# Kernel tuning notes

Measured on AMD Instinct MI355X. Metric: run time of the kernel, lower is better.

Reference implementation:

```python
import jax, jax.numpy as jnp
import numpy as np

B, N, C, H = 1, 4096, 768, 12
HD = C // H  # 64
EPS = 1e-5


def _rope_freqs(n, hd, theta=10000.0):
    inv = 1.0 / (theta ** (np.arange(0, hd, 2, dtype=np.float32) / hd))  # (hd/2,)
    ang = np.outer(np.arange(n, dtype=np.float32), inv)  # (N, hd/2)
    return jnp.asarray(np.cos(ang)), jnp.asarray(np.sin(ang))


def setup_inputs() -> dict:
    key = jax.random.key(0)
    ks = jax.random.split(key, 5)
    cos, sin = _rope_freqs(N, HD)
    s = lambda d: 1.0 / np.sqrt(d)
    return {
        "x": jax.random.normal(ks[0], (B, N, C), jnp.float32),
        "freqs_cos": cos,
        "freqs_sin": sin,
        "w_qkv": jax.random.normal(ks[1], (3 * C, C), jnp.float32) * s(C),
        "w_proj": jax.random.normal(ks[2], (C, C), jnp.float32) * s(C),
        "b_proj": jnp.zeros((C,), jnp.float32),
        "g1": jnp.ones((C,), jnp.float32),
        "beta1": jnp.zeros((C,), jnp.float32),
        "g2": jnp.ones((C,), jnp.float32),
        "beta2": jnp.zeros((C,), jnp.float32),
        "w_fc1": jax.random.normal(ks[3], (4 * C, C), jnp.float32) * s(C),
        "b_fc1": jnp.zeros((4 * C,), jnp.float32),
        "w_fc2": jax.random.normal(ks[4], (C, 4 * C), jnp.float32) * s(4 * C),
        "b_fc2": jnp.zeros((C,), jnp.float32),
    }


def _layernorm(x, g, b):
    mu = jnp.mean(x, -1, keepdims=True)
    var = jnp.mean(jnp.square(x - mu), -1, keepdims=True)
    return (x - mu) * jax.lax.rsqrt(var + EPS) * g + b


def _apply_rope(t, cos, sin):
    # t: (B, N, H, HD); cos/sin: (N, HD/2) -> broadcast (1, N, 1, HD/2)
    t = t.reshape(*t.shape[:-1], HD // 2, 2)
    t0, t1 = t[..., 0], t[..., 1]
    c = cos[None, :, None, :]
    s = sin[None, :, None, :]
    out = jnp.stack([t0 * c - t1 * s, t0 * s + t1 * c], axis=-1)
    return out.reshape(*out.shape[:-2], HD)


def reference(x, freqs_cos, freqs_sin, w_qkv, w_proj, b_proj, g1, beta1, g2, beta2,
              w_fc1, b_fc1, w_fc2, b_fc2):
    # --- attention branch ---
    h = _layernorm(x, g1, beta1)
    qkv = (h @ w_qkv.T).reshape(B, N, 3, H, HD)
    q, k, v = qkv[:, :, 0], qkv[:, :, 1], qkv[:, :, 2]  # (B,N,H,HD)
    q = _apply_rope(q, freqs_cos, freqs_sin)
    k = _apply_rope(k, freqs_cos, freqs_sin)
    scale = HD ** (-0.5)
    attn = jnp.einsum('bnhd,bmhd->bhnm', q, k) * scale
    attn = jax.nn.softmax(attn, axis=-1)
    o = jnp.einsum('bhnm,bmhd->bnhd', attn, v).reshape(B, N, C)
    x = x + o @ w_proj.T + b_proj
    # --- mlp branch ---
    h = _layernorm(x, g2, beta2)
    h = jax.nn.gelu(h @ w_fc1.T + b_fc1, approximate=False)
    x = x + h @ w_fc2.T + b_fc2
    return x
```

## Files before the change

### kernel.cpp

```cpp
#include <hip/hip_runtime.h>
#include <hip/hip_bf16.h>
#include <math.h>

#define LOG2E 1.44269504088896340736f

typedef short bf16x8 __attribute__((ext_vector_type(8)));
typedef float f32x4 __attribute__((ext_vector_type(4)));

static __device__ __forceinline__ float bf2f(ushort u){
  union { float f; unsigned int u; } x; x.u = ((unsigned int)u) << 16; return x.f;
}
static __device__ __forceinline__ ushort f2bf(float f){
  union { float f; unsigned int u; } x; x.f = f;
  unsigned int r = x.u + 0x7fffu + ((x.u >> 16) & 1u);
  return (ushort)(r >> 16);
}
static __device__ __forceinline__ unsigned cvt_pk_bf16(float a, float b){
  unsigned r;
  asm("v_cvt_pk_bf16_f32 %0, %1, %2" : "=v"(r) : "v"(a), "v"(b));
  return r;
}
static __device__ __forceinline__ float fmax3(float a, float b, float c){
  return fmaxf(fmaxf(a, b), c);
}
static __device__ __forceinline__ void gload_lds16(const void* g, void* l){
  __builtin_amdgcn_global_load_lds(
      (const __attribute__((address_space(1))) unsigned int*)g,
      (__attribute__((address_space(3))) unsigned int*)l, 16, 0, 0);
}

__global__ __launch_bounds__(256) void cvt_f32_bf16(const float* __restrict__ src,
                                                    ushort* __restrict__ dst, int n4){
  int i = blockIdx.x * 256 + threadIdx.x;
  if (i < n4){
    float4 v = ((const float4*)src)[i];
    ushort4 o;
    o.x = f2bf(v.x); o.y = f2bf(v.y); o.z = f2bf(v.z); o.w = f2bf(v.w);
    ((ushort4*)dst)[i] = o;
  }
}

__device__ __forceinline__ float block_sum256(float s, float* red){
  #pragma unroll
  for (int off = 32; off; off >>= 1) s += __shfl_xor(s, off, 64);
  int w = threadIdx.x >> 6;
  if ((threadIdx.x & 63) == 0) red[w] = s;
  __syncthreads();
  float tot = red[0] + red[1] + red[2] + red[3];
  __syncthreads();
  return tot;
}

__global__ __launch_bounds__(256) void ln_kernel(const float* __restrict__ x,
                                                 const float* __restrict__ g,
                                                 const float* __restrict__ bta,
                                                 ushort* __restrict__ out){
  __shared__ float red[4];
  int row = blockIdx.x, t = threadIdx.x;
  const float* xr = x + (size_t)row * 768;
  float v0 = xr[t], v1 = xr[t + 256], v2 = xr[t + 512];
  float mu = block_sum256(v0 + v1 + v2, red) * (1.0f / 768.0f);
  float d0 = v0 - mu, d1 = v1 - mu, d2 = v2 - mu;
  float var = block_sum256(d0*d0 + d1*d1 + d2*d2, red) * (1.0f / 768.0f);
  float rs = rsqrtf(var + 1e-5f);
  ushort* orow = out + (size_t)row * 768;
  orow[t]       = f2bf(d0 * rs * g[t]       + bta[t]);
  orow[t + 256] = f2bf(d1 * rs * g[t + 256] + bta[t + 256]);
  orow[t + 512] = f2bf(d2 * rs * g[t + 512] + bta[t + 512]);
}

template<int MODE>
__global__ __launch_bounds__(256) void gemm_bf16(const ushort* __restrict__ A, int lda,
                                                 const ushort* __restrict__ Bm, int ldb,
                                                 int K,
                                                 const float* __restrict__ bias,
                                                 const float* __restrict__ res, int ldr,
                                                 void* __restrict__ out, int ldo){
  __shared__ __align__(16) ushort As[128 * 64];
  __shared__ __align__(16) ushort Bs[128 * 64];
  const int tid = threadIdx.x;
  const int m0 = blockIdx.x * 128, n0 = blockIdx.y * 128;
  const int w = tid >> 6, l = tid & 63;
  const int wm = (w >> 1) * 64, wn = (w & 1) * 64;
  const int lr = l & 15, lg = l >> 4;
  const int lane8 = l >> 3, sl = l & 7;
  const int koff = (MODE == 3) ? blockIdx.z * K : 0;

  f32x4 acc[4][4] = {};

  for (int k0 = 0; k0 < K; k0 += 64){
    #pragma unroll
    for (int j = 0; j < 4; ++j){
      int instr = w * 4 + j;
      int row = instr * 8 + lane8;
      gload_lds16((const char*)A + ((size_t)(m0 + row) * lda + koff + k0) * 2 + ((sl ^ (row & 7)) << 4),
                  (char*)As + instr * 1024);
      gload_lds16((const char*)Bm + ((size_t)(n0 + row) * ldb + koff + k0) * 2 + ((sl ^ (row & 7)) << 4),
                  (char*)Bs + instr * 1024);
    }
    __syncthreads();
    #pragma unroll
    for (int kk = 0; kk < 2; ++kk){
      bf16x8 af[4], bfr[4];
      #pragma unroll
      for (int mi = 0; mi < 4; ++mi){
        int row = wm + mi * 16 + lr;
        int cg = (kk * 4 + lg) ^ (row & 7);
        af[mi] = *(const bf16x8*)(As + row * 64 + cg * 8);
      }
      #pragma unroll
      for (int nj = 0; nj < 4; ++nj){
        int row = wn + nj * 16 + lr;
        int cg = (kk * 4 + lg) ^ (row & 7);
        bfr[nj] = *(const bf16x8*)(Bs + row * 64 + cg * 8);
      }
      #pragma unroll
      for (int mi = 0; mi < 4; ++mi)
        #pragma unroll
        for (int nj = 0; nj < 4; ++nj)
          acc[mi][nj] = __builtin_amdgcn_mfma_f32_16x16x32_bf16(af[mi], bfr[nj], acc[mi][nj], 0, 0, 0);
    }
    __syncthreads();
  }

  const size_t zout = (MODE == 3) ? (size_t)blockIdx.z * gridDim.x * 128 * ldo : 0;

  #pragma unroll
  for (int mi = 0; mi < 4; ++mi){
    #pragma unroll
    for (int nj = 0; nj < 4; ++nj){
      #pragma unroll
      for (int r = 0; r < 4; ++r){
        int grow = m0 + wm + mi * 16 + lg * 4 + r;
        int gcol = n0 + wn + nj * 16 + lr;
        float v = acc[mi][nj][r];
        if (MODE == 0){
          ((ushort*)out)[(size_t)grow * ldo + gcol] = f2bf(v);
        } else if (MODE == 1){
          v += bias[gcol] + res[(size_t)grow * ldr + gcol];
          ((float*)out)[(size_t)grow * ldo + gcol] = v;
        } else if (MODE == 2){
          v += bias[gcol];
          v = 0.5f * v * (1.0f + erff(v * 0.70710678118654752f));
          ((ushort*)out)[(size_t)grow * ldo + gcol] = f2bf(v);
        } else {
          ((float*)out)[zout + (size_t)grow * ldo + gcol] = v;
        }
      }
    }
  }
}

__global__ __launch_bounds__(192) void gemm_combine4(const float* __restrict__ parts,
                                                     const float* __restrict__ bias,
                                                     const float* __restrict__ res,
                                                     float* __restrict__ out){
  int q = blockIdx.x, t = threadIdx.x;
  size_t idx = (size_t)q * 768 + t * 4;
  const size_t seg = (size_t)4096 * 768;
  f32x4 o = *(const f32x4*)(parts + idx);
  #pragma unroll
  for (int s = 1; s < 4; ++s) o += *(const f32x4*)(parts + s * seg + idx);
  f32x4 b = *(const f32x4*)(bias + t * 4);
  f32x4 rr = *(const f32x4*)(res + idx);
  o += b + rr;
  *(f32x4*)(out + idx) = o;
}

__global__ __launch_bounds__(384) void rope_kernel(const ushort* __restrict__ qkv,
                                                   const float* __restrict__ fc,
                                                   const float* __restrict__ fs,
                                                   ushort* __restrict__ Qs,
                                                   ushort* __restrict__ Ks,
                                                   ushort* __restrict__ Vt){
  int n = blockIdx.x, t = threadIdx.x;
  int h = t >> 5, p = t & 31;
  float c = fc[(size_t)n * 32 + p], s = fs[(size_t)n * 32 + p];
  const ushort* row = qkv + (size_t)n * 2304;
  const float qscale = 0.125f * LOG2E;
  {
    float t0 = bf2f(row[h * 64 + 2 * p]), t1 = bf2f(row[h * 64 + 2 * p + 1]);
    ushort* dst = Qs + ((size_t)h * 4096 + n) * 64;
    dst[2 * p]     = f2bf((t0 * c - t1 * s) * qscale);
    dst[2 * p + 1] = f2bf((t0 * s + t1 * c) * qscale);
  }
  {
    float t0 = bf2f(row[768 + h * 64 + 2 * p]), t1 = bf2f(row[768 + h * 64 + 2 * p + 1]);
    ushort* dst = Ks + ((size_t)h * 4096 + n) * 64;
    dst[2 * p]     = f2bf(t0 * c - t1 * s);
    dst[2 * p + 1] = f2bf(t0 * s + t1 * c);
  }
  #pragma unroll
  for (int i = 0; i < 2; ++i){
    int idx = t + i * 384;
    int hh = idx >> 6, d = idx & 63;
    Vt[((size_t)hh * 64 + d) * 4096 + n] = row[1536 + idx];
  }
}

__global__ __launch_bounds__(256, 4) void flash_attn(const ushort* __restrict__ Qs,
                                                     const ushort* __restrict__ Ks,
                                                     const ushort* __restrict__ Vt,
                                                     float* __restrict__ Opart,
                                                     float* __restrict__ Ml){
  __shared__ __align__(16) char smem[32768];
  const int h = blockIdx.y, kh = blockIdx.z;
  const int w = threadIdx.x >> 6, l = threadIdx.x & 63;
  const int lr = l & 15, lg = l >> 4;
  const int lane8 = l >> 3, sl = l & 7;
  const int q0 = blockIdx.x * 128 + w * 32;
  const ushort* Qh = Qs + (size_t)h * (4096 * 64);
  const char* Kh = (const char*)(Ks + (size_t)h * (4096 * 64));
  const char* Vh = (const char*)(Vt + (size_t)h * (64 * 4096));

  bf16x8 qa[2][2];
  #pragma unroll
  for (int qf = 0; qf < 2; ++qf)
    #pragma unroll
    for (int kk = 0; kk < 2; ++kk)
      qa[qf][kk] = *(const bf16x8*)(Qh + (size_t)(q0 + qf * 16 + lr) * 64 + kk * 32 + lg * 8);

  const char* kbase = Kh + (size_t)(kh * 1024 + w * 16 + lane8) * 128;
  const char* vbase = Vh + (size_t)(w * 16 + lane8) * 8192 + kh * 2048 + ((sl ^ lane8) << 4);
  int koff[2];
  #pragma unroll
  for (int j = 0; j < 2; ++j)
    koff[j] = j * 1024 + ((sl ^ ((lane8 & 3) | (((w * 2 + j) & 1) << 2))) << 4);

  const int a_ = lr >> 2, b_ = lr & 3;
  const int krow = 8 * a_ + b_;
  const int f_ = b_ | ((a_ & 1) << 2);
  const int kslot0 = (lg ^ f_) << 4;
  const int kslot1 = ((4 + lg) ^ f_) << 4;
  const int vslot0 = lr * 128 + ((lg ^ (lr & 7)) << 4);
  const int vslot1 = lr * 128 + (((4 + lg) ^ (lr & 7)) << 4);

  f32x4 oacc[2][4] = {};
  f32x4 lacc[2] = {};
  float m_prev[2] = {0.0f, 0.0f};
  union { unsigned u[4]; bf16x8 v; } ones;
  #pragma unroll
  for (int i = 0; i < 4; ++i) ones.u[i] = 0x3F803F80u;

  auto stage = [&](int tile, char* Kb, char* Vb){
    #pragma unroll
    for (int j = 0; j < 2; ++j){
      gload_lds16(kbase + (size_t)tile * 8192 + koff[j], Kb + (w * 2 + j) * 1024);
      gload_lds16(vbase + (size_t)j * 65536 + (size_t)tile * 128, Vb + (w * 2 + j) * 1024);
    }
  };

  auto compute = [&](const char* Kb, const char* Vb, bool first){
    #pragma unroll
    for (int kk = 0; kk < 2; ++kk){
      const bool fst = first && (kk == 0);
      f32x4 sh[2][2];
      #pragma unroll
      for (int qf = 0; qf < 2; ++qf){
        float iv = fst ? 0.0f : -m_prev[qf];
        #pragma unroll
        for (int tt = 0; tt < 2; ++tt){
          sh[qf][tt][0] = iv; sh[qf][tt][1] = iv; sh[qf][tt][2] = iv; sh[qf][tt][3] = iv;
        }
      }
      #pragma unroll
      for (int tt = 0; tt < 2; ++tt){
        const char* kr = Kb + (krow + 4 * tt + 32 * kk) * 128;
        bf16x8 k0 = *(const bf16x8*)(kr + kslot0);
        bf16x8 k1 = *(const bf16x8*)(kr + kslot1);
        #pragma unroll
        for (int qf = 0; qf < 2; ++qf){
          sh[qf][tt] = __builtin_amdgcn_mfma_f32_16x16x32_bf16(k0, qa[qf][0], sh[qf][tt], 0, 0, 0);
          sh[qf][tt] = __builtin_amdgcn_mfma_f32_16x16x32_bf16(k1, qa[qf][1], sh[qf][tt], 0, 0, 0);
        }
      }
      float mb[2];
      #pragma unroll
      for (int qf = 0; qf < 2; ++qf){
        float m1 = fmax3(sh[qf][0][0], sh[qf][0][1], sh[qf][0][2]);
        float m2 = fmax3(sh[qf][0][3], sh[qf][1][0], sh[qf][1][1]);
        float m3 = fmaxf(sh[qf][1][2], sh[qf][1][3]);
        float mm = fmax3(m1, m2, m3);
        mm = fmaxf(mm, __shfl_xor(mm, 16, 64));
        mm = fmaxf(mm, __shfl_xor(mm, 32, 64));
        mb[qf] = mm;
      }
      if (fst){
        #pragma unroll
        for (int qf = 0; qf < 2; ++qf){
          m_prev[qf] = mb[qf];
          #pragma unroll
          for (int tt = 0; tt < 2; ++tt)
            #pragma unroll
            for (int r = 0; r < 4; ++r) sh[qf][tt][r] -= mb[qf];
        }
      } else if (!__all(mb[0] <= 8.0f && mb[1] <= 8.0f)){
        #pragma unroll
        for (int qf = 0; qf < 2; ++qf){
          float d = (mb[qf] > 8.0f) ? mb[qf] : 0.0f;
          float sc = exp2f(-d);
          #pragma unroll
          for (int tt = 0; tt < 2; ++tt)
            #pragma unroll
            for (int r = 0; r < 4; ++r) sh[qf][tt][r] -= d;
          #pragma unroll
          for (int db = 0; db < 4; ++db)
            #pragma unroll
            for (int r = 0; r < 4; ++r) oacc[qf][db][r] *= sc;
          #pragma unroll
          for (int r = 0; r < 4; ++r) lacc[qf][r] *= sc;
          m_prev[qf] += d;
        }
      }
      #pragma unroll
      for (int qf = 0; qf < 2; ++qf)
        #pragma unroll
        for (int tt = 0; tt < 2; ++tt)
          #pragma unroll
          for (int r = 0; r < 4; ++r)
            sh[qf][tt][r] = exp2f(sh[qf][tt][r]);
      union { unsigned u[4]; bf16x8 v; } pf[2];
      #pragma unroll
      for (int qf = 0; qf < 2; ++qf){
        pf[qf].u[0] = cvt_pk_bf16(sh[qf][0][0], sh[qf][0][1]);
        pf[qf].u[1] = cvt_pk_bf16(sh[qf][0][2], sh[qf][0][3]);
        pf[qf].u[2] = cvt_pk_bf16(sh[qf][1][0], sh[qf][1][1]);
        pf[qf].u[3] = cvt_pk_bf16(sh[qf][1][2], sh[qf][1][3]);
      }
      const int vs = kk ? vslot1 : vslot0;
      #pragma unroll
      for (int db = 0; db < 4; ++db){
        bf16x8 vf = *(const bf16x8*)(Vb + vs + db * 2048);
        #pragma unroll
        for (int qf = 0; qf < 2; ++qf)
          oacc[qf][db] = __builtin_amdgcn_mfma_f32_16x16x32_bf16(vf, pf[qf].v, oacc[qf][db], 0, 0, 0);
      }
      #pragma unroll
      for (int qf = 0; qf < 2; ++qf)
        lacc[qf] = __builtin_amdgcn_mfma_f32_16x16x32_bf16(ones.v, pf[qf].v, lacc[qf], 0, 0, 0);
    }
  };

  char* K0 = smem;          char* V0 = smem + 8192;
  char* K1 = smem + 16384;  char* V1 = smem + 24576;

  stage(0, K0, V0);
  __syncthreads();
  stage(1, K1, V1);
  compute(K0, V0, true);
  __syncthreads();
  stage(2, K0, V0);
  compute(K1, V1, false);
  __syncthreads();
  #pragma unroll 1
  for (int it2 = 1; it2 < 8; ++it2){
    stage(2 * it2 + 1, K1, V1);
    compute(K0, V0, false);
    __syncthreads();
    if (it2 < 7) stage(2 * it2 + 2, K0, V0);
    compute(K1, V1, false);
    __syncthreads();
  }

  #pragma unroll
  for (int qf = 0; qf < 2; ++qf){
    int q = q0 + qf * 16 + lr;
    float* Op = Opart + ((size_t)(kh * 12 + h) * 4096 + q) * 64;
    #pragma unroll
    for (int db = 0; db < 4; ++db)
      *(f32x4*)(Op + db * 16 + 4 * lg) = oacc[qf][db];
    if (lg == 0){
      float2 ml; ml.x = m_prev[qf]; ml.y = lacc[qf][0];
      *(float2*)(Ml + ((size_t)(kh * 12 + h) * 4096 + q) * 2) = ml;
    }
  }
}

__global__ __launch_bounds__(192) void attn_combine(const float* __restrict__ Opart,
                                                    const float* __restrict__ Ml,
                                                    ushort* __restrict__ O){
  int q = blockIdx.x, t = threadIdx.x;
  int h = t >> 4;
  float2 ml[4];
  float m = -1e30f;
  #pragma unroll
  for (int s = 0; s < 4; ++s){
    ml[s] = *(const float2*)(Ml + ((size_t)(s * 12 + h) * 4096 + q) * 2);
    m = fmaxf(m, ml[s].x);
  }
  float wgt[4], lsum = 0.0f;
  #pragma unroll
  for (int s = 0; s < 4; ++s){
    wgt[s] = exp2f(ml[s].x - m);
    lsum += ml[s].y * wgt[s];
  }
  float inv = 1.0f / lsum;
  int dd = (t & 15) * 4;
  f32x4 o = {};
  #pragma unroll
  for (int s = 0; s < 4; ++s){
    f32x4 os = *(const f32x4*)(Opart + ((size_t)(s * 12 + h) * 4096 + q) * 64 + dd);
    #pragma unroll
    for (int r = 0; r < 4; ++r) o[r] += os[r] * wgt[s];
  }
  uint2 ov;
  ov.x = cvt_pk_bf16(o[0] * inv, o[1] * inv);
  ov.y = cvt_pk_bf16(o[2] * inv, o[3] * inv);
  *(uint2*)(O + (size_t)q * 768 + t * 4) = ov;
}

extern "C" void kernel_launch(void* const* d_in, const int* in_sizes, int n_in,
                              void* d_out, int out_size, void* d_ws, size_t ws_size,
                              hipStream_t stream){
  const float* x      = (const float*)d_in[0];
  const float* fcos   = (const float*)d_in[1];
  const float* fsin   = (const float*)d_in[2];
  const float* w_qkv  = (const float*)d_in[3];
  const float* w_proj = (const float*)d_in[4];
  const float* b_proj = (const float*)d_in[5];
  const float* g1     = (const float*)d_in[6];
  const float* beta1  = (const float*)d_in[7];
  const float* g2     = (const float*)d_in[8];
  const float* beta2  = (const float*)d_in[9];
  const float* w_fc1  = (const float*)d_in[10];
  const float* b_fc1  = (const float*)d_in[11];
  const float* w_fc2  = (const float*)d_in[12];
  const float* b_fc2  = (const float*)d_in[13];

  char* ws = (char*)d_ws;
  size_t off = 0;
  auto alloc = [&](size_t bytes) -> char* {
    char* p = ws + off; off += (bytes + 255) & ~(size_t)255; return p;
  };
  ushort* wq  = (ushort*)alloc((size_t)2304 * 768 * 2);
  ushort* wp  = (ushort*)alloc((size_t)768 * 768 * 2);
  ushort* w1  = (ushort*)alloc((size_t)3072 * 768 * 2);
  ushort* w2  = (ushort*)alloc((size_t)768 * 3072 * 2);
  ushort* h1  = (ushort*)alloc((size_t)4096 * 768 * 2);
  ushort* qkv = (ushort*)alloc((size_t)4096 * 2304 * 2);
  ushort* Qs  = (ushort*)alloc((size_t)12 * 4096 * 64 * 2);
  ushort* Ks  = (ushort*)alloc((size_t)12 * 4096 * 64 * 2);
  ushort* Vt  = (ushort*)alloc((size_t)12 * 64 * 4096 * 2);
  ushort* ao  = (ushort*)alloc((size_t)4096 * 768 * 2);
  float*  x2  = (float*) alloc((size_t)4096 * 768 * 4);
  ushort* h2  = (ushort*)alloc((size_t)4096 * 768 * 2);
  ushort* f1  = (ushort*)alloc((size_t)4096 * 3072 * 2);
  float*  Opart = (float*)alloc((size_t)4 * 12 * 4096 * 64 * 4);
  float*  Ml    = (float*)alloc((size_t)4 * 12 * 4096 * 2 * 4);
  float*  skp   = Opart;

  cvt_f32_bf16<<<(2304*768/4 + 255)/256, 256, 0, stream>>>(w_qkv,  wq, 2304*768/4);
  cvt_f32_bf16<<<(768*768/4  + 255)/256, 256, 0, stream>>>(w_proj, wp, 768*768/4);
  cvt_f32_bf16<<<(3072*768/4 + 255)/256, 256, 0, stream>>>(w_fc1,  w1, 3072*768/4);
  cvt_f32_bf16<<<(768*3072/4 + 255)/256, 256, 0, stream>>>(w_fc2,  w2, 768*3072/4);

  ln_kernel<<<4096, 256, 0, stream>>>(x, g1, beta1, h1);
  gemm_bf16<0><<<dim3(32, 18), 256, 0, stream>>>(h1, 768, wq, 768, 768,
                                                 nullptr, nullptr, 0, qkv, 2304);
  rope_kernel<<<4096, 384, 0, stream>>>(qkv, fcos, fsin, Qs, Ks, Vt);
  flash_attn<<<dim3(32, 12, 4), 256, 0, stream>>>(Qs, Ks, Vt, Opart, Ml);
  attn_combine<<<4096, 192, 0, stream>>>(Opart, Ml, ao);
  gemm_bf16<3><<<dim3(32, 6, 4), 256, 0, stream>>>(ao, 768, wp, 768, 192,
                                                   nullptr, nullptr, 0, skp, 768);
  gemm_combine4<<<4096, 192, 0, stream>>>(skp, b_proj, x, x2);
  ln_kernel<<<4096, 256, 0, stream>>>(x2, g2, beta2, h2);
  gemm_bf16<2><<<dim3(32, 24), 256, 0, stream>>>(h2, 768, w1, 768, 768,
                                                 b_fc1, nullptr, 0, f1, 3072);
  gemm_bf16<3><<<dim3(32, 6, 4), 256, 0, stream>>>(f1, 3072, w2, 3072, 768,
                                                   nullptr, nullptr, 0, skp, 768);
  gemm_combine4<<<4096, 192, 0, stream>>>(skp, b_fc2, x2, (float*)d_out);
}
```

Before: 278.9 us.

## Fuse RoPE into QKV GEMM epilogue, merge weight casts, warp-per-row layernorm

The four weight conversion launches become one kernel. Layernorm now runs one row per wavefront with vector loads and no shared-memory reductions. The QKV GEMM gains an epilogue that applies RoPE through a DPP lane swap and writes Q, K and transposed V directly, so the separate rope kernel and the qkv intermediate buffer are gone. The output-projection GEMM drops split-K plus its combine pass and uses a fused bias-plus-residual epilogue. Flash attention computes the full 64-key score tile before a single max reduction, which halves the cross-lane reductions but keeps more registers live and launches fewer blocks for the projection.

```diff
diff --git a/kernel.cpp b/kernel.cpp
--- a/kernel.cpp
+++ b/kernel.cpp
@@ -23,50 +23,72 @@
 static __device__ __forceinline__ float fmax3(float a, float b, float c){
   return fmaxf(fmaxf(a, b), c);
 }
+static __device__ __forceinline__ float dpp_xor1(float v){
+  int i = __builtin_amdgcn_mov_dpp(__float_as_int(v), 0xB1, 0xF, 0xF, true);
+  return __int_as_float(i);
+}
 static __device__ __forceinline__ void gload_lds16(const void* g, void* l){
   __builtin_amdgcn_global_load_lds(
       (const __attribute__((address_space(1))) unsigned int*)g,
       (__attribute__((address_space(3))) unsigned int*)l, 16, 0, 0);
 }
 
-__global__ __launch_bounds__(256) void cvt_f32_bf16(const float* __restrict__ src,
-                                                    ushort* __restrict__ dst, int n4){
-  int i = blockIdx.x * 256 + threadIdx.x;
-  if (i < n4){
-    float4 v = ((const float4*)src)[i];
-    ushort4 o;
-    o.x = f2bf(v.x); o.y = f2bf(v.y); o.z = f2bf(v.z); o.w = f2bf(v.w);
-    ((ushort4*)dst)[i] = o;
-  }
-}
-
-__device__ __forceinline__ float block_sum256(float s, float* red){
-  #pragma unroll
-  for (int off = 32; off; off >>= 1) s += __shfl_xor(s, off, 64);
-  int w = threadIdx.x >> 6;
-  if ((threadIdx.x & 63) == 0) red[w] = s;
-  __syncthreads();
-  float tot = red[0] + red[1] + red[2] + red[3];
-  __syncthreads();
-  return tot;
+__global__ __launch_bounds__(256) void cvt_all(const float* __restrict__ s0, ushort* __restrict__ d0, int c0,
+                                               const float* __restrict__ s1, ushort* __restrict__ d1, int c1,
+                                               const float* __restrict__ s2, ushort* __restrict__ d2, int c2,
+                                               const float* __restrict__ s3, ushort* __restrict__ d3, int c3){
+  int j = blockIdx.x * 256 + threadIdx.x;
+  const float* s; ushort* d;
+  if (j < c0){ s = s0; d = d0; }
+  else { j -= c0;
+    if (j < c1){ s = s1; d = d1; }
+    else { j -= c1;
+      if (j < c2){ s = s2; d = d2; }
+      else { j -= c2; if (j >= c3) return; s = s3; d = d3; } } }
+  float4 v = ((const float4*)s)[j];
+  ushort4 o;
+  o.x = f2bf(v.x); o.y = f2bf(v.y); o.z = f2bf(v.z); o.w = f2bf(v.w);
+  ((ushort4*)d)[j] = o;
 }
 
 __global__ __launch_bounds__(256) void ln_kernel(const float* __restrict__ x,
                                                  const float* __restrict__ g,
                                                  const float* __restrict__ bta,
                                                  ushort* __restrict__ out){
-  __shared__ float red[4];
-  int row = blockIdx.x, t = threadIdx.x;
+  int w = threadIdx.x >> 6, l = threadIdx.x & 63;
+  int row = blockIdx.x * 4 + w;
   const float* xr = x + (size_t)row * 768;
-  float v0 = xr[t], v1 = xr[t + 256], v2 = xr[t + 512];
-  float mu = block_sum256(v0 + v1 + v2, red) * (1.0f / 768.0f);
-  float d0 = v0 - mu, d1 = v1 - mu, d2 = v2 - mu;
-  float var = block_sum256(d0*d0 + d1*d1 + d2*d2, red) * (1.0f / 768.0f);
-  float rs = rsqrtf(var + 1e-5f);
+  f32x4 v[3];
+  #pragma unroll
+  for (int i = 0; i < 3; ++i) v[i] = *(const f32x4*)(xr + i * 256 + l * 4);
+  float s = 0.0f;
+  #pragma unroll
+  for (int i = 0; i < 3; ++i)
+    #pragma unroll
+    for (int r = 0; r < 4; ++r) s += v[i][r];
+  #pragma unroll
+  for (int off = 32; off; off >>= 1) s += __shfl_xor(s, off, 64);
+  float mu = s * (1.0f / 768.0f);
+  float q = 0.0f;
+  #pragma unroll
+  for (int i = 0; i < 3; ++i)
+    #pragma unroll
+    for (int r = 0; r < 4; ++r){ float d = v[i][r] - mu; q += d * d; }
+  #pragma unroll
+  for (int off = 32; off; off >>= 1) q += __shfl_xor(q, off, 64);
+  float rs = rsqrtf(q * (1.0f / 768.0f) + 1e-5f);
   ushort* orow = out + (size_t)row * 768;
-  orow[t]       = f2bf(d0 * rs * g[t]       + bta[t]);
-  orow[t + 256] = f2bf(d1 * rs * g[t + 256] + bta[t + 256]);
-  orow[t + 512] = f2bf(d2 * rs * g[t + 512] + bta[t + 512]);
+  #pragma unroll
+  for (int i = 0; i < 3; ++i){
+    f32x4 gg = *(const f32x4*)(g + i * 256 + l * 4);
+    f32x4 bb = *(const f32x4*)(bta + i * 256 + l * 4);
+    ushort4 o;
+    o.x = f2bf((v[i][0] - mu) * rs * gg[0] + bb[0]);
+    o.y = f2bf((v[i][1] - mu) * rs * gg[1] + bb[1]);
+    o.z = f2bf((v[i][2] - mu) * rs * gg[2] + bb[2]);
+    o.w = f2bf((v[i][3] - mu) * rs * gg[3] + bb[3]);
+    *(ushort4*)(orow + i * 256 + l * 4) = o;
+  }
 }
 
 template<int MODE>
@@ -75,7 +97,12 @@
                                                  int K,
                                                  const float* __restrict__ bias,
                                                  const float* __restrict__ res, int ldr,
-                                                 void* __restrict__ out, int ldo){
+                                                 void* __restrict__ out, int ldo,
+                                                 const float* __restrict__ fc,
+                                                 const float* __restrict__ fs,
+                                                 ushort* __restrict__ Qs,
+                                                 ushort* __restrict__ Ks,
+                                                 ushort* __restrict__ Vt){
   __shared__ __align__(16) ushort As[128 * 64];
   __shared__ __align__(16) ushort Bs[128 * 64];
   const int tid = threadIdx.x;
@@ -124,6 +151,42 @@
   }
 
   const size_t zout = (MODE == 3) ? (size_t)blockIdx.z * gridDim.x * 128 * ldo : 0;
+
+  if (MODE == 4){
+    const int part = n0 / 768;
+    const float qsc = 0.125f * LOG2E;
+    #pragma unroll
+    for (int mi = 0; mi < 4; ++mi){
+      const int n_base = m0 + wm + mi * 16 + lg * 4;
+      #pragma unroll
+      for (int nj = 0; nj < 4; ++nj){
+        const int col = n0 + wn + nj * 16 + lr;
+        const int head = (col - part * 768) >> 6;
+        const int d = col & 63;
+        if (part == 2){
+          ushort4 pk;
+          pk.x = f2bf(acc[mi][nj][0]); pk.y = f2bf(acc[mi][nj][1]);
+          pk.z = f2bf(acc[mi][nj][2]); pk.w = f2bf(acc[mi][nj][3]);
+          *(ushort4*)(Vt + ((size_t)head * 64 + d) * 4096 + n_base) = pk;
+        } else {
+          const int p = d >> 1;
+          ushort* dst = (part == 0) ? Qs : Ks;
+          #pragma unroll
+          for (int r = 0; r < 4; ++r){
+            int n = n_base + r;
+            float v = acc[mi][nj][r];
+            float pv = dpp_xor1(v);
+            float c = fc[(size_t)n * 32 + p];
+            float sv = fs[(size_t)n * 32 + p];
+            float rr = v * c + pv * ((d & 1) ? sv : -sv);
+            if (part == 0) rr *= qsc;
+            dst[((size_t)head * 4096 + n) * 64 + d] = f2bf(rr);
+          }
+        }
+      }
+    }
+    return;
+  }
 
   #pragma unroll
   for (int mi = 0; mi < 4; ++mi){
@@ -167,37 +230,6 @@
   *(f32x4*)(out + idx) = o;
 }
 
-__global__ __launch_bounds__(384) void rope_kernel(const ushort* __restrict__ qkv,
-                                                   const float* __restrict__ fc,
-                                                   const float* __restrict__ fs,
-                                                   ushort* __restrict__ Qs,
-                                                   ushort* __restrict__ Ks,
-                                                   ushort* __restrict__ Vt){
-  int n = blockIdx.x, t = threadIdx.x;
-  int h = t >> 5, p = t & 31;
-  float c = fc[(size_t)n * 32 + p], s = fs[(size_t)n * 32 + p];
-  const ushort* row = qkv + (size_t)n * 2304;
-  const float qscale = 0.125f * LOG2E;
-  {
-    float t0 = bf2f(row[h * 64 + 2 * p]), t1 = bf2f(row[h * 64 + 2 * p + 1]);
-    ushort* dst = Qs + ((size_t)h * 4096 + n) * 64;
-    dst[2 * p]     = f2bf((t0 * c - t1 * s) * qscale);
-    dst[2 * p + 1] = f2bf((t0 * s + t1 * c) * qscale);
-  }
-  {
-    float t0 = bf2f(row[768 + h * 64 + 2 * p]), t1 = bf2f(row[768 + h * 64 + 2 * p + 1]);
-    ushort* dst = Ks + ((size_t)h * 4096 + n) * 64;
-    dst[2 * p]     = f2bf(t0 * c - t1 * s);
-    dst[2 * p + 1] = f2bf(t0 * s + t1 * c);
-  }
-  #pragma unroll
-  for (int i = 0; i < 2; ++i){
-    int idx = t + i * 384;
-    int hh = idx >> 6, d = idx & 63;
-    Vt[((size_t)hh * 64 + d) * 4096 + n] = row[1536 + idx];
-  }
-}
-
 __global__ __launch_bounds__(256, 4) void flash_attn(const ushort* __restrict__ Qs,
                                                      const ushort* __restrict__ Ks,
                                                      const ushort* __restrict__ Vt,
@@ -251,81 +283,83 @@
   };
 
   auto compute = [&](const char* Kb, const char* Vb, bool first){
+    f32x4 sh[2][4];
+    #pragma unroll
+    for (int qf = 0; qf < 2; ++qf){
+      float iv = first ? 0.0f : -m_prev[qf];
+      #pragma unroll
+      for (int t = 0; t < 4; ++t){
+        sh[qf][t][0] = iv; sh[qf][t][1] = iv; sh[qf][t][2] = iv; sh[qf][t][3] = iv;
+      }
+    }
+    #pragma unroll
+    for (int t = 0; t < 4; ++t){
+      const char* kr = Kb + (krow + 4 * (t & 1) + 32 * (t >> 1)) * 128;
+      bf16x8 k0 = *(const bf16x8*)(kr + kslot0);
+      bf16x8 k1 = *(const bf16x8*)(kr + kslot1);
+      #pragma unroll
+      for (int qf = 0; qf < 2; ++qf){
+        sh[qf][t] = __builtin_amdgcn_mfma_f32_16x16x32_bf16(k0, qa[qf][0], sh[qf][t], 0, 0, 0);
+        sh[qf][t] = __builtin_amdgcn_mfma_f32_16x16x32_bf16(k1, qa[qf][1], sh[qf][t], 0, 0, 0);
+      }
+    }
+    float mb[2];
+    #pragma unroll
+    for (int qf = 0; qf < 2; ++qf){
+      float m1 = fmax3(sh[qf][0][0], sh[qf][0][1], sh[qf][0][2]);
+      float m2 = fmax3(sh[qf][0][3], sh[qf][1][0], sh[qf][1][1]);
+      float m3 = fmax3(sh[qf][1][2], sh[qf][1][3], sh[qf][2][0]);
+      float m4 = fmax3(sh[qf][2][1], sh[qf][2][2], sh[qf][2][3]);
+      float m5 = fmax3(sh[qf][3][0], sh[qf][3][1], sh[qf][3][2]);
+      mb[qf] = fmax3(fmaxf(m1, m2), fmax3(m3, m4, m5), sh[qf][3][3]);
+    }
+    if (first){
+      #pragma unroll
+      for (int qf = 0; qf < 2; ++qf){
+        float mm = fmaxf(mb[qf], __shfl_xor(mb[qf], 16, 64));
+        mm = fmaxf(mm, __shfl_xor(mm, 32, 64));
+        m_prev[qf] = mm;
+        #pragma unroll
+        for (int t = 0; t < 4; ++t)
+          #pragma unroll
+          for (int r = 0; r < 4; ++r) sh[qf][t][r] -= mm;
+      }
+    } else if (!__all(mb[0] <= 8.0f && mb[1] <= 8.0f)){
+      #pragma unroll
+      for (int qf = 0; qf < 2; ++qf){
+        float mm = fmaxf(mb[qf], __shfl_xor(mb[qf], 16, 64));
+        mm = fmaxf(mm, __shfl_xor(mm, 32, 64));
+        float d = (mm > 8.0f) ? mm : 0.0f;
+        float sc = exp2f(-d);
+        #pragma unroll
+        for (int t = 0; t < 4; ++t)
+          #pragma unroll
+          for (int r = 0; r < 4; ++r) sh[qf][t][r] -= d;
+        #pragma unroll
+        for (int db = 0; db < 4; ++db)
+          #pragma unroll
+          for (int r = 0; r < 4; ++r) oacc[qf][db][r] *= sc;
+        #pragma unroll
+        for (int r = 0; r < 4; ++r) lacc[qf][r] *= sc;
+        m_prev[qf] += d;
+      }
+    }
+    #pragma unroll
+    for (int qf = 0; qf < 2; ++qf)
+      #pragma unroll
+      for (int t = 0; t < 4; ++t)
+        #pragma unroll
+        for (int r = 0; r < 4; ++r)
+          sh[qf][t][r] = exp2f(sh[qf][t][r]);
     #pragma unroll
     for (int kk = 0; kk < 2; ++kk){
-      const bool fst = first && (kk == 0);
-      f32x4 sh[2][2];
+      union { unsigned u[4]; bf16x8 v; } pf[2];
       #pragma unroll
       for (int qf = 0; qf < 2; ++qf){
-        float iv = fst ? 0.0f : -m_prev[qf];
-        #pragma unroll
-        for (int tt = 0; tt < 2; ++tt){
-          sh[qf][tt][0] = iv; sh[qf][tt][1] = iv; sh[qf][tt][2] = iv; sh[qf][tt][3] = iv;
-        }
-      }
-      #pragma unroll
-      for (int tt = 0; tt < 2; ++tt){
-        const char* kr = Kb + (krow + 4 * tt + 32 * kk) * 128;
-        bf16x8 k0 = *(const bf16x8*)(kr + kslot0);
-        bf16x8 k1 = *(const bf16x8*)(kr + kslot1);
-        #pragma unroll
-        for (int qf = 0; qf < 2; ++qf){
-          sh[qf][tt] = __builtin_amdgcn_mfma_f32_16x16x32_bf16(k0, qa[qf][0], sh[qf][tt], 0, 0, 0);
-          sh[qf][tt] = __builtin_amdgcn_mfma_f32_16x16x32_bf16(k1, qa[qf][1], sh[qf][tt], 0, 0, 0);
-        }
-      }
-      float mb[2];
-      #pragma unroll
-      for (int qf = 0; qf < 2; ++qf){
-        float m1 = fmax3(sh[qf][0][0], sh[qf][0][1], sh[qf][0][2]);
-        float m2 = fmax3(sh[qf][0][3], sh[qf][1][0], sh[qf][1][1]);
-        float m3 = fmaxf(sh[qf][1][2], sh[qf][1][3]);
-        float mm = fmax3(m1, m2, m3);
-        mm = fmaxf(mm, __shfl_xor(mm, 16, 64));
-        mm = fmaxf(mm, __shfl_xor(mm, 32, 64));
-        mb[qf] = mm;
-      }
-      if (fst){
-        #pragma unroll
-        for (int qf = 0; qf < 2; ++qf){
-          m_prev[qf] = mb[qf];
-          #pragma unroll
-          for (int tt = 0; tt < 2; ++tt)
-            #pragma unroll
-            for (int r = 0; r < 4; ++r) sh[qf][tt][r] -= mb[qf];
-        }
-      } else if (!__all(mb[0] <= 8.0f && mb[1] <= 8.0f)){
-        #pragma unroll
-        for (int qf = 0; qf < 2; ++qf){
-          float d = (mb[qf] > 8.0f) ? mb[qf] : 0.0f;
-          float sc = exp2f(-d);
-          #pragma unroll
-          for (int tt = 0; tt < 2; ++tt)
-            #pragma unroll
-            for (int r = 0; r < 4; ++r) sh[qf][tt][r] -= d;
-          #pragma unroll
-          for (int db = 0; db < 4; ++db)
-            #pragma unroll
-            for (int r = 0; r < 4; ++r) oacc[qf][db][r] *= sc;
-          #pragma unroll
-          for (int r = 0; r < 4; ++r) lacc[qf][r] *= sc;
-          m_prev[qf] += d;
-        }
-      }
-      #pragma unroll
-      for (int qf = 0; qf < 2; ++qf)
-        #pragma unroll
-        for (int tt = 0; tt < 2; ++tt)
-          #pragma unroll
-          for (int r = 0; r < 4; ++r)
-            sh[qf][tt][r] = exp2f(sh[qf][tt][r]);
-      union { unsigned u[4]; bf16x8 v; } pf[2];
-      #pragma unroll
-      for (int qf = 0; qf < 2; ++qf){
-        pf[qf].u[0] = cvt_pk_bf16(sh[qf][0][0], sh[qf][0][1]);
-        pf[qf].u[1] = cvt_pk_bf16(sh[qf][0][2], sh[qf][0][3]);
-        pf[qf].u[2] = cvt_pk_bf16(sh[qf][1][0], sh[qf][1][1]);
-        pf[qf].u[3] = cvt_pk_bf16(sh[qf][1][2], sh[qf][1][3]);
+        pf[qf].u[0] = cvt_pk_bf16(sh[qf][2*kk][0],   sh[qf][2*kk][1]);
+        pf[qf].u[1] = cvt_pk_bf16(sh[qf][2*kk][2],   sh[qf][2*kk][3]);
+        pf[qf].u[2] = cvt_pk_bf16(sh[qf][2*kk+1][0], sh[qf][2*kk+1][1]);
+        pf[qf].u[3] = cvt_pk_bf16(sh[qf][2*kk+1][2], sh[qf][2*kk+1][3]);
       }
       const int vs = kk ? vslot1 : vslot0;
       #pragma unroll
@@ -437,7 +471,6 @@
   ushort* w1  = (ushort*)alloc((size_t)3072 * 768 * 2);
   ushort* w2  = (ushort*)alloc((size_t)768 * 3072 * 2);
   ushort* h1  = (ushort*)alloc((size_t)4096 * 768 * 2);
-  ushort* qkv = (ushort*)alloc((size_t)4096 * 2304 * 2);
   ushort* Qs  = (ushort*)alloc((size_t)12 * 4096 * 64 * 2);
   ushort* Ks  = (ushort*)alloc((size_t)12 * 4096 * 64 * 2);
   ushort* Vt  = (ushort*)alloc((size_t)12 * 64 * 4096 * 2);
@@ -449,24 +482,25 @@
   float*  Ml    = (float*)alloc((size_t)4 * 12 * 4096 * 2 * 4);
   float*  skp   = Opart;
 
-  cvt_f32_bf16<<<(2304*768/4 + 255)/256, 256, 0, stream>>>(w_qkv,  wq, 2304*768/4);
-  cvt_f32_bf16<<<(768*768/4  + 255)/256, 256, 0, stream>>>(w_proj, wp, 768*768/4);
-  cvt_f32_bf16<<<(3072*768/4 + 255)/256, 256, 0, stream>>>(w_fc1,  w1, 3072*768/4);
-  cvt_f32_bf16<<<(768*3072/4 + 255)/256, 256, 0, stream>>>(w_fc2,  w2, 768*3072/4);
-
-  ln_kernel<<<4096, 256, 0, stream>>>(x, g1, beta1, h1);
-  gemm_bf16<0><<<dim3(32, 18), 256, 0, stream>>>(h1, 768, wq, 768, 768,
-                                                 nullptr, nullptr, 0, qkv, 2304);
-  rope_kernel<<<4096, 384, 0, stream>>>(qkv, fcos, fsin, Qs, Ks, Vt);
+  const int c0 = 2304*768/4, c1 = 768*768/4, c2 = 3072*768/4, c3 = 768*3072/4;
+  cvt_all<<<(c0 + c1 + c2 + c3 + 255)/256, 256, 0, stream>>>(
+      w_qkv, wq, c0, w_proj, wp, c1, w_fc1, w1, c2, w_fc2, w2, c3);
+
+  ln_kernel<<<1024, 256, 0, stream>>>(x, g1, beta1, h1);
+  gemm_bf16<4><<<dim3(32, 18), 256, 0, stream>>>(h1, 768, wq, 768, 768,
+                                                 nullptr, nullptr, 0, nullptr, 0,
+                                                 fcos, fsin, Qs, Ks, Vt);
   flash_attn<<<dim3(32, 12, 4), 256, 0, stream>>>(Qs, Ks, Vt, Opart, Ml);
   attn_combine<<<4096, 192, 0, stream>>>(Opart, Ml, ao);
-  gemm_bf16<3><<<dim3(32, 6, 4), 256, 0, stream>>>(ao, 768, wp, 768, 192,
-                                                   nullptr, nullptr, 0, skp, 768);
-  gemm_combine4<<<4096, 192, 0, stream>>>(skp, b_proj, x, x2);
-  ln_kernel<<<4096, 256, 0, stream>>>(x2, g2, beta2, h2);
+  gemm_bf16<1><<<dim3(32, 6), 256, 0, stream>>>(ao, 768, wp, 768, 768,
+                                                b_proj, x, 768, x2, 768,
+                                                nullptr, nullptr, nullptr, nullptr, nullptr);
+  ln_kernel<<<1024, 256, 0, stream>>>(x2, g2, beta2, h2);
   gemm_bf16<2><<<dim3(32, 24), 256, 0, stream>>>(h2, 768, w1, 768, 768,
-                                                 b_fc1, nullptr, 0, f1, 3072);
+                                                 b_fc1, nullptr, 0, f1, 3072,
+                                                 nullptr, nullptr, nullptr, nullptr, nullptr);
   gemm_bf16<3><<<dim3(32, 6, 4), 256, 0, stream>>>(f1, 3072, w2, 3072, 768,
-                                                   nullptr, nullptr, 0, skp, 768);
+                                                   nullptr, nullptr, 0, skp, 768,
+                                                   nullptr, nullptr, nullptr, nullptr, nullptr);
   gemm_combine4<<<4096, 192, 0, stream>>>(skp, b_fc2, x2, (float*)d_out);
 }
```

Result: faster. 244.1 us (-12.5%).
